# Performance work log

Hardware: AMD Instinct MI355X
Metric: run time of the kernel (lower is better)

## Reference

```python
import jax, jax.numpy as jnp
import numpy as np

# static config (matches init_kwargs)
T_K = 3      # Time_kernel
K = 3        # spatial_kernel_side_length
C = 64       # dim_hidden
H = 4        # num_head
D = 16       # dim_head
NL = 2       # num_layers
F = 3        # dim_feature
N, S1, S2 = 32, 32, 32
P = K // 2
L1 = T_K // 2
M = T_K * K * K
EPS = 1e-5


def _neighbor_mask():
    # spatial_neighbor_mask with an all-ones city mask: offset (k1,k2) is a valid
    # neighbor of cell (s1,s2) iff it lands inside the grid.
    m = np.zeros((S1, S2, K, K), dtype=bool)
    s1 = np.arange(S1); s2 = np.arange(S2)
    for k1 in range(K):
        v1 = (s1 + k1 - P >= 0) & (s1 + k1 - P < S1)
        for k2 in range(K):
            v2 = (s2 + k2 - P >= 0) & (s2 + k2 - P < S2)
            m[:, :, k1, k2] = v1[:, None] & v2[None, :]
    mf = m.reshape(S1, S2, K * K)
    # tiled across Time_kernel, flattened in (t, k1, k2) order like the torch code
    return np.tile(mf[:, :, None, :], (1, 1, T_K, 1)).reshape(S1, S2, M)

_MASK = jnp.asarray(_neighbor_mask())


def _forward(x, W_in, b_in, W_out, b_out, Wq, bq, Wk, bk, Wv, bv):
    # BatchNorm2d (training-mode batch stats, affine = identity init)
    mean = x.mean(axis=(0, 1, 2))
    var = ((x - mean) ** 2).mean(axis=(0, 1, 2))
    h = (x - mean) * jax.lax.rsqrt(var + EPS)
    h = h @ W_in + b_in  # [N,S1,S2,C]

    for l in range(NL):
        res = h  # res_block_thickness = 1 -> residual every layer
        q = (h @ Wq[l] + bq[l]).reshape(N, S1, S2, H, D)
        # spatial unfold (nn.Unfold, padding=K//2, stride=1)
        hp = jnp.pad(h, ((0, 0), (P, P), (P, P), (0, 0)))
        u = jnp.stack([jnp.stack([hp[:, k1:k1 + S1, k2:k2 + S2, :]
                                  for k2 in range(K)]) for k1 in range(K)])  # [K,K,N,S1,S2,C]
        # time unfold (zero-padded shifts along N)
        up = jnp.pad(u, ((0, 0), (0, 0), (L1, L1), (0, 0), (0, 0), (0, 0)))
        ut = jnp.stack([up[:, :, t:t + N] for t in range(T_K)])  # [T,K,K,N,S1,S2,C]
        # per-offset single-Linear MLPs (kernel_neurons=[C,C]), batched over T,K,K
        ks = jnp.einsum('tijnabc,tijcd->nabtijd', ut, Wk[l]) + bk[l]
        vs = jnp.einsum('tijnabc,tijcd->nabtijd', ut, Wv[l]) + bv[l]
        kM = ks.reshape(N, S1, S2, M, H, D)
        vM = vs.reshape(N, S1, S2, M, H, D)
        # unscaled dot-product attention over valid neighbors (masked == dropped)
        sc = jnp.einsum('nabmhd,nabhd->nabhm', kM, q)
        sc = jnp.where(_MASK[None, :, :, None, :], sc, -1e30)
        w = jax.nn.softmax(sc, axis=-1)
        h = jnp.einsum('nabhm,nabmhd->nabhd', w, vM).reshape(N, S1, S2, C)
        h = h + res

    return h @ W_out + b_out  # [N,S1,S2,F]


def setup_inputs() -> dict:
    key = jax.random.key(0)
    k = jax.random.split(key, 11)
    s = 0.05
    return {
        'x': jax.random.normal(k[0], (N, S1, S2, F), jnp.float32),
        'W_in': jax.random.normal(k[1], (F, C), jnp.float32) * s,
        'b_in': jax.random.normal(k[2], (C,), jnp.float32) * s,
        'W_out': jax.random.normal(k[3], (C, F), jnp.float32) * s,
        'b_out': jax.random.normal(k[4], (F,), jnp.float32) * s,
        'Wq': jax.random.normal(k[5], (NL, C, C), jnp.float32) * s,
        'bq': jax.random.normal(k[6], (NL, C), jnp.float32) * s,
        'Wk': jax.random.normal(k[7], (NL, T_K, K, K, C, C), jnp.float32) * s,
        'bk': jax.random.normal(k[8], (NL, T_K, K, K, C), jnp.float32) * s,
        'Wv': jax.random.normal(k[9], (NL, T_K, K, K, C, C), jnp.float32) * s,
        'bv': jax.random.normal(k[10], (NL, T_K, K, K, C), jnp.float32) * s,
    }


def reference(x, W_in, b_in, W_out, b_out, Wq, bq, Wk, bk, Wv, bv):
    return _forward(x, W_in, b_in, W_out, b_out, Wq, bq, Wk, bk, Wv, bv)
```

## Files before the change

### kernel.cpp

```cpp
#include <hip/hip_runtime.h>
#include <hip/hip_bf16.h>


typedef short short8_t __attribute__((ext_vector_type(8)));
typedef float floatx4 __attribute__((ext_vector_type(4)));

__device__ __forceinline__ short f2bs(float f) {
    __hip_bfloat16 h = __float2bfloat16(f);
    return *reinterpret_cast<short*>(&h);
}
__device__ __forceinline__ float bs2f(short s) {
    union { unsigned u; float f; } v;
    v.u = ((unsigned)(unsigned short)s) << 16;
    return v.f;
}
__device__ __forceinline__ int hn_idx(int rowid, int chunk) {
    return rowid * 64 + ((chunk ^ (rowid & 7)) << 3);
}
__device__ __forceinline__ float quad_sum(float p) {
    float a = p, b = p;
    asm("v_permlane16_swap_b32 %0, %1" : "+v"(a), "+v"(b));
    float s = a + b;
    float c = s, d = s;
    asm("v_permlane32_swap_b32 %0, %1" : "+v"(c), "+v"(d));
    return c + d;
}

__global__ void prep_kernel(const float* __restrict__ Wq, const float* __restrict__ Wk,
                            const float* __restrict__ Wv, short* __restrict__ dst,
                            const float* __restrict__ x, float* __restrict__ sums) {
    if (blockIdx.x < 220) {
        int t = blockIdx.x * 256 + threadIdx.x;
        if (t >= 110 * 512) return;
        int mat  = t >> 9;
        int rem  = t & 511;
        int kk   = rem >> 8;
        int nt   = (rem >> 6) & 3;
        int lane = rem & 63;
        int krow = kk * 32 + (lane >> 4) * 8;
        int col  = nt * 16 + (lane & 15);
        const float* W;
        if (mat < 2)       W = Wq + mat * 4096;
        else if (mat < 56) W = Wk + (mat - 2) * 4096;
        else               W = Wv + (mat - 56) * 4096;
        short8_t v;
        #pragma unroll
        for (int j = 0; j < 8; ++j) v[j] = f2bs(W[(krow + j) * 64 + col]);
        *(short8_t*)&dst[(size_t)mat * 4096 + ((kk * 4 + nt) * 64 + lane) * 8] = v;
    } else {
        int bid = blockIdx.x - 220;
        int t = bid * 256 + threadIdx.x;
        const float4* x4 = (const float4*)x;
        float4 v0 = x4[t * 3 + 0], v1 = x4[t * 3 + 1], v2 = x4[t * 3 + 2];
        float vv[6];
        vv[0] = v0.x + v0.w + v1.z + v2.y;
        vv[1] = v0.y + v1.x + v1.w + v2.z;
        vv[2] = v0.z + v1.y + v2.x + v2.w;
        vv[3] = v0.x*v0.x + v0.w*v0.w + v1.z*v1.z + v2.y*v2.y;
        vv[4] = v0.y*v0.y + v1.x*v1.x + v1.w*v1.w + v2.z*v2.z;
        vv[5] = v0.z*v0.z + v1.y*v1.y + v2.x*v2.x + v2.w*v2.w;
        #pragma unroll
        for (int i = 0; i < 6; ++i) {
            #pragma unroll
            for (int off = 1; off < 64; off <<= 1) vv[i] += __shfl_xor(vv[i], off);
        }
        __shared__ float part[4][6];
        if ((threadIdx.x & 63) == 0) {
            #pragma unroll
            for (int i = 0; i < 6; ++i) part[threadIdx.x >> 6][i] = vv[i];
        }
        __syncthreads();
        if (threadIdx.x < 6)
            sums[bid * 8 + threadIdx.x] = part[0][threadIdx.x] + part[1][threadIdx.x] +
                                          part[2][threadIdx.x] + part[3][threadIdx.x];
    }
}

template <bool FIRST>
__global__ __launch_bounds__(512, 4)
void layer_fused(const float* __restrict__ x, const float* __restrict__ sums,
                 const float* __restrict__ W_in, const float* __restrict__ b_in,
                 const short* __restrict__ hbf_in, short* __restrict__ hbf_out,
                 const float* __restrict__ Wout, const float* __restrict__ bout,
                 float* __restrict__ out,
                 const short* __restrict__ wqB, const float* __restrict__ bq,
                 const short* __restrict__ wkB, const float* __restrict__ bk,
                 const short* __restrict__ wvB, const float* __restrict__ bv) {
    __shared__ short HnS[216 * 64];
    __shared__ float Waux[256];
    __shared__ float bn6[6];

    const int tid = threadIdx.x;
    const int bb0 = blockIdx.x * 2, a = blockIdx.y, nb = blockIdx.z;

    if (FIRST) {
        if (tid < 3) {
            float s = 0.f, qq = 0.f;
            #pragma unroll
            for (int p = 0; p < 32; ++p) { s += sums[p * 8 + tid]; qq += sums[p * 8 + 3 + tid]; }
            float mean = s * (1.f / 32768.f);
            float var  = qq * (1.f / 32768.f) - mean * mean;
            bn6[tid]     = mean;
            bn6[3 + tid] = rsqrtf(var + 1e-5f);
        }
        if (tid < 192)      Waux[tid] = W_in[tid];
        else if (tid < 256) Waux[tid] = b_in[tid - 192];
    } else {
        if (tid < 192)      Waux[tid] = Wout[tid];
        else if (tid < 195) Waux[tid] = bout[tid - 192];
    }
    __syncthreads();

    float mean0 = 0, mean1 = 0, mean2 = 0, rs0 = 0, rs1 = 0, rs2 = 0;
    if (FIRST) {
        mean0 = bn6[0]; mean1 = bn6[1]; mean2 = bn6[2];
        rs0 = bn6[3]; rs1 = bn6[4]; rs2 = bn6[5];
    }

    for (int id = tid; id < 1728; id += 512) {
        int rowid = id >> 3, cc = id & 7;
        int r = rowid % 18;
        int rw = rowid / 18;
        int spa = rw >> 2, jcol = rw & 3;
        int aa = a + spa - 1, bb = bb0 + jcol - 1;
        int n  = nb * 16 + r - 1;
        short8_t v = {0, 0, 0, 0, 0, 0, 0, 0};
        if ((unsigned)n < 32u && (unsigned)aa < 32u && (unsigned)bb < 32u) {
            int cell = (n * 32 + aa) * 32 + bb;
            if (FIRST) {
                float xn0 = (x[cell*3+0] - mean0) * rs0;
                float xn1 = (x[cell*3+1] - mean1) * rs1;
                float xn2 = (x[cell*3+2] - mean2) * rs2;
                #pragma unroll
                for (int j = 0; j < 8; ++j) {
                    int c = cc * 8 + j;
                    float h = Waux[192+c] + xn0*Waux[c] + xn1*Waux[64+c] + xn2*Waux[128+c];
                    v[j] = f2bs(h);
                }
            } else {
                v = *(const short8_t*)&hbf_in[cell * 64 + cc * 8];
            }
        }
        *(short8_t*)&HnS[hn_idx(rowid, cc)] = v;
    }
    __syncthreads();

    const int lane = tid & 63;
    const int wv8  = tid >> 6;
    const int w    = wv8 & 3;
    const int g2   = wv8 >> 2;
    const int e    = lane & 15;
    const int q    = lane >> 4;
    const int c0   = w * 16 + q * 4;

    bool va[3], vb[4];
    #pragma unroll
    for (int d = 0; d < 3; ++d) va[d] = (unsigned)(a + d - 1) < 32u;
    #pragma unroll
    for (int j = 0; j < 4; ++j) vb[j] = (unsigned)(bb0 + j - 1) < 32u;

    floatx4 qv[2];
    {
        short8_t wq0 = *(const short8_t*)&wqB[((0 * 4 + w) * 64 + lane) * 8];
        short8_t wq1 = *(const short8_t*)&wqB[((1 * 4 + w) * 64 + lane) * 8];
        const float4 bq4 = *(const float4*)&bq[c0];
        #pragma unroll
        for (int ci = 0; ci < 2; ++ci) {
            const int row = (5 + ci) * 18 + e + 1;
            short8_t h0 = *(const short8_t*)&HnS[hn_idx(row, q)];
            short8_t h1 = *(const short8_t*)&HnS[hn_idx(row, 4 + q)];
            floatx4 acc = {bq4.x, bq4.y, bq4.z, bq4.w};
            acc = __builtin_amdgcn_mfma_f32_16x16x32_bf16(wq0, h0, acc, 0, 0, 0);
            acc = __builtin_amdgcn_mfma_f32_16x16x32_bf16(wq1, h1, acc, 0, 0, 0);
            qv[ci] = acc;
        }
    }

    floatx4 o[2] = {{0,0,0,0},{0,0,0,0}};
    float ss[2] = {0.f, 0.f};

    const int mstart = g2 ? 14 : 0;
    const int mend   = g2 ? 27 : 14;
    for (int m = mstart; m < mend; ++m) {
        const int t  = (m * 57) >> 9;
        const int sp = m - 9 * t;
        const int di = (sp * 11) >> 5;
        const int dj = sp - 3 * di;
        if (!va[di]) continue;
        short8_t wk0 = *(const short8_t*)&wkB[m * 4096 + ((0 * 4 + w) * 64 + lane) * 8];
        short8_t wk1 = *(const short8_t*)&wkB[m * 4096 + ((1 * 4 + w) * 64 + lane) * 8];
        short8_t wv0 = *(const short8_t*)&wvB[m * 4096 + ((0 * 4 + w) * 64 + lane) * 8];
        short8_t wv1 = *(const short8_t*)&wvB[m * 4096 + ((1 * 4 + w) * 64 + lane) * 8];
        const float4 bk4 = *(const float4*)&bk[m * 64 + c0];
        const float4 bv4 = *(const float4*)&bv[m * 64 + c0];
        const int rowb = (di * 4 + dj) * 18 + e + t;
        #pragma unroll
        for (int ci = 0; ci < 2; ++ci) {
            if (!vb[dj + ci]) continue;
            const int row = rowb + ci * 18;
            short8_t h0 = *(const short8_t*)&HnS[hn_idx(row, q)];
            short8_t h1 = *(const short8_t*)&HnS[hn_idx(row, 4 + q)];
            floatx4 kacc = {bk4.x, bk4.y, bk4.z, bk4.w};
            kacc = __builtin_amdgcn_mfma_f32_16x16x32_bf16(wk0, h0, kacc, 0, 0, 0);
            kacc = __builtin_amdgcn_mfma_f32_16x16x32_bf16(wk1, h1, kacc, 0, 0, 0);
            floatx4 vacc = {bv4.x, bv4.y, bv4.z, bv4.w};
            vacc = __builtin_amdgcn_mfma_f32_16x16x32_bf16(wv0, h0, vacc, 0, 0, 0);
            vacc = __builtin_amdgcn_mfma_f32_16x16x32_bf16(wv1, h1, vacc, 0, 0, 0);
            float p = kacc[0] * qv[ci][0] + kacc[1] * qv[ci][1]
                    + kacc[2] * qv[ci][2] + kacc[3] * qv[ci][3];
            p = quad_sum(p);
            float wgt = __expf(p);
            ss[ci] += wgt;
            o[ci][0] += wgt * vacc[0];
            o[ci][1] += wgt * vacc[1];
            o[ci][2] += wgt * vacc[2];
            o[ci][3] += wgt * vacc[3];
        }
    }

    __syncthreads();
    float* stbuf = (float*)HnS;
    if (g2 == 1) {
        #pragma unroll
        for (int ci = 0; ci < 2; ++ci) {
            float* d = &stbuf[(((w * 64 + lane) * 2) + ci) * 5];
            d[0] = ss[ci];
            d[1] = o[ci][0]; d[2] = o[ci][1]; d[3] = o[ci][2]; d[4] = o[ci][3];
        }
    }
    __syncthreads();
    if (g2 == 0) {
        #pragma unroll
        for (int ci = 0; ci < 2; ++ci) {
            const float* d = &stbuf[(((w * 64 + lane) * 2) + ci) * 5];
            float inv = 1.0f / (ss[ci] + d[0]);
            o[ci][0] = (o[ci][0] + d[1]) * inv;
            o[ci][1] = (o[ci][1] + d[2]) * inv;
            o[ci][2] = (o[ci][2] + d[3]) * inv;
            o[ci][3] = (o[ci][3] + d[4]) * inv;
        }
    }

    const int n = nb * 16 + e;
    if (FIRST) {
        if (g2 == 0) {
            #pragma unroll
            for (int ci = 0; ci < 2; ++ci) {
                int cell = (n * 32 + a) * 32 + bb0 + ci;
                float xn0 = (x[cell*3+0] - mean0) * rs0;
                float xn1 = (x[cell*3+1] - mean1) * rs1;
                float xn2 = (x[cell*3+2] - mean2) * rs2;
                short4 hb; short* hbp = (short*)&hb;
                #pragma unroll
                for (int i = 0; i < 4; ++i) {
                    int c = c0 + i;
                    float res = Waux[192+c] + xn0*Waux[c] + xn1*Waux[64+c] + xn2*Waux[128+c];
                    hbp[i] = f2bs(o[ci][i] + res);
                }
                *(short4*)&hbf_out[cell * 64 + c0] = hb;
            }
        }
    } else {
        __syncthreads();
        float* hf = (float*)HnS;
        if (g2 == 0) {
            #pragma unroll
            for (int ci = 0; ci < 2; ++ci) {
                int cell = (n * 32 + a) * 32 + bb0 + ci;
                short4 hb = *(const short4*)&hbf_in[cell * 64 + c0];
                float* d = &hf[(ci * 16 + e) * 65 + c0];
                d[0] = o[ci][0] + bs2f(hb.x);
                d[1] = o[ci][1] + bs2f(hb.y);
                d[2] = o[ci][2] + bs2f(hb.z);
                d[3] = o[ci][3] + bs2f(hb.w);
            }
        }
        __syncthreads();
        if (tid < 96) {
            int rowglob = tid / 3, f = tid - rowglob * 3;
            int ci = rowglob >> 4, row = rowglob & 15;
            float acc = Waux[192 + f];
            #pragma unroll 8
            for (int cc = 0; cc < 64; ++cc) acc += hf[rowglob * 65 + cc] * Waux[cc * 3 + f];
            int nn = nb * 16 + row;
            out[((nn * 32 + a) * 32 + bb0 + ci) * 3 + f] = acc;
        }
    }
}

extern "C" void kernel_launch(void* const* d_in, const int* in_sizes, int n_in,
                              void* d_out, int out_size, void* d_ws, size_t ws_size,
                              hipStream_t stream) {
    const float* x     = (const float*)d_in[0];
    const float* W_in  = (const float*)d_in[1];
    const float* b_in  = (const float*)d_in[2];
    const float* W_out = (const float*)d_in[3];
    const float* b_out = (const float*)d_in[4];
    const float* Wq    = (const float*)d_in[5];
    const float* bq    = (const float*)d_in[6];
    const float* Wk    = (const float*)d_in[7];
    const float* bk    = (const float*)d_in[8];
    const float* Wv    = (const float*)d_in[9];
    const float* bv    = (const float*)d_in[10];

    float* ws    = (float*)d_ws;
    float* sums  = ws;
    short* h1bf  = (short*)(ws + 256);
    short* wB    = h1bf + 2097152;
    float* out   = (float*)d_out;

    prep_kernel<<<252, 256, 0, stream>>>(Wq, Wk, Wv, wB, x, sums);

    const short* wq0 = wB;                const short* wq1 = wB + 4096;
    const short* wk0 = wB + 2 * 4096;     const short* wk1 = wB + (2 + 27) * 4096;
    const short* wv0 = wB + 56 * 4096;    const short* wv1 = wB + (56 + 27) * 4096;

    dim3 grid(16, 32, 2);
    layer_fused<true><<<grid, 512, 0, stream>>>(
        x, sums, W_in, b_in, nullptr, h1bf, nullptr, nullptr, nullptr,
        wq0, bq, wk0, bk, wv0, bv);
    layer_fused<false><<<grid, 512, 0, stream>>>(
        nullptr, nullptr, nullptr, nullptr, h1bf, nullptr, W_out, b_out, out,
        wq1, bq + 64, wk1, bk + 1728, wv1, bv + 1728);
}
```

Baseline: 144.9 us.

## Switch attention MFMAs to 32x32x16 tiles with four-way offset split

```diff
diff --git a/kernel.cpp b/kernel.cpp
--- a/kernel.cpp
+++ b/kernel.cpp
@@ -3,7 +3,7 @@
 
 
 typedef short short8_t __attribute__((ext_vector_type(8)));
-typedef float floatx4 __attribute__((ext_vector_type(4)));
+typedef float floatx16 __attribute__((ext_vector_type(16)));
 
 __device__ __forceinline__ short f2bs(float f) {
     __hip_bfloat16 h = __float2bfloat16(f);
@@ -17,13 +17,10 @@
 __device__ __forceinline__ int hn_idx(int rowid, int chunk) {
     return rowid * 64 + ((chunk ^ (rowid & 7)) << 3);
 }
-__device__ __forceinline__ float quad_sum(float p) {
+__device__ __forceinline__ float half_sum(float p) {
     float a = p, b = p;
-    asm("v_permlane16_swap_b32 %0, %1" : "+v"(a), "+v"(b));
-    float s = a + b;
-    float c = s, d = s;
-    asm("v_permlane32_swap_b32 %0, %1" : "+v"(c), "+v"(d));
-    return c + d;
+    asm("v_permlane32_swap_b32 %0, %1" : "+v"(a), "+v"(b));
+    return a + b;
 }
 
 __global__ void prep_kernel(const float* __restrict__ Wq, const float* __restrict__ Wk,
@@ -34,11 +31,11 @@
         if (t >= 110 * 512) return;
         int mat  = t >> 9;
         int rem  = t & 511;
-        int kk   = rem >> 8;
-        int nt   = (rem >> 6) & 3;
+        int hp   = rem >> 8;
+        int kk   = (rem >> 6) & 3;
         int lane = rem & 63;
-        int krow = kk * 32 + (lane >> 4) * 8;
-        int col  = nt * 16 + (lane & 15);
+        int krow = kk * 16 + ((lane >> 5) << 3);
+        int col  = hp * 32 + (lane & 31);
         const float* W;
         if (mat < 2)       W = Wq + mat * 4096;
         else if (mat < 56) W = Wk + (mat - 2) * 4096;
@@ -46,7 +43,7 @@
         short8_t v;
         #pragma unroll
         for (int j = 0; j < 8; ++j) v[j] = f2bs(W[(krow + j) * 64 + col]);
-        *(short8_t*)&dst[(size_t)mat * 4096 + ((kk * 4 + nt) * 64 + lane) * 8] = v;
+        *(short8_t*)&dst[(size_t)mat * 4096 + ((hp * 4 + kk) * 64 + lane) * 8] = v;
     } else {
         int bid = blockIdx.x - 220;
         int t = bid * 256 + threadIdx.x;
@@ -77,7 +74,7 @@
 }
 
 template <bool FIRST>
-__global__ __launch_bounds__(512, 4)
+__global__ __launch_bounds__(512, 2)
 void layer_fused(const float* __restrict__ x, const float* __restrict__ sums,
                  const float* __restrict__ W_in, const float* __restrict__ b_in,
                  const short* __restrict__ hbf_in, short* __restrict__ hbf_out,
@@ -147,143 +144,203 @@
 
     const int lane = tid & 63;
     const int wv8  = tid >> 6;
-    const int w    = wv8 & 3;
-    const int g2   = wv8 >> 2;
-    const int e    = lane & 15;
-    const int q    = lane >> 4;
-    const int c0   = w * 16 + q * 4;
-
-    bool va[3], vb[4];
+    const int hp   = wv8 & 1;
+    const int g4   = wv8 >> 1;
+    const int col  = lane & 31;
+    const int e    = col & 15;
+    const int ci   = col >> 4;
+    const int h5   = lane >> 5;
+
+    unsigned amask = 0;
     #pragma unroll
-    for (int d = 0; d < 3; ++d) va[d] = (unsigned)(a + d - 1) < 32u;
-    #pragma unroll
-    for (int j = 0; j < 4; ++j) vb[j] = (unsigned)(bb0 + j - 1) < 32u;
-
-    floatx4 qv[2];
+    for (int d = 0; d < 3; ++d) if ((unsigned)(a + d - 1) < 32u) amask |= 1u << d;
+    const bool vbL = (unsigned)(bb0 - 1) < 32u;
+    const bool vbR = (unsigned)(bb0 + 2) < 32u;
+    const unsigned vmask = (ci == 0) ? ((vbL ? 1u : 0u) | 2u | 4u)
+                                     : (1u | 2u | (vbR ? 4u : 0u));
+
+    const int elane = e + ci * 18;
+
+    floatx16 qv;
     {
-        short8_t wq0 = *(const short8_t*)&wqB[((0 * 4 + w) * 64 + lane) * 8];
-        short8_t wq1 = *(const short8_t*)&wqB[((1 * 4 + w) * 64 + lane) * 8];
-        const float4 bq4 = *(const float4*)&bq[c0];
-        #pragma unroll
-        for (int ci = 0; ci < 2; ++ci) {
-            const int row = (5 + ci) * 18 + e + 1;
-            short8_t h0 = *(const short8_t*)&HnS[hn_idx(row, q)];
-            short8_t h1 = *(const short8_t*)&HnS[hn_idx(row, 4 + q)];
-            floatx4 acc = {bq4.x, bq4.y, bq4.z, bq4.w};
-            acc = __builtin_amdgcn_mfma_f32_16x16x32_bf16(wq0, h0, acc, 0, 0, 0);
-            acc = __builtin_amdgcn_mfma_f32_16x16x32_bf16(wq1, h1, acc, 0, 0, 0);
-            qv[ci] = acc;
-        }
-    }
-
-    floatx4 o[2] = {{0,0,0,0},{0,0,0,0}};
-    float ss[2] = {0.f, 0.f};
-
-    const int mstart = g2 ? 14 : 0;
-    const int mend   = g2 ? 27 : 14;
+        const float* bqp = &bq[hp * 32 + 4 * h5];
+        const float4 qa = *(const float4*)&bqp[0];
+        const float4 qb = *(const float4*)&bqp[8];
+        const float4 qc = *(const float4*)&bqp[16];
+        const float4 qd = *(const float4*)&bqp[24];
+        qv = floatx16{qa.x,qa.y,qa.z,qa.w, qb.x,qb.y,qb.z,qb.w,
+                      qc.x,qc.y,qc.z,qc.w, qd.x,qd.y,qd.z,qd.w};
+        const int hrow = (5 + ci) * 18 + e + 1;
+        const int hb = hrow * 64, xr = hrow & 7;
+        const short8_t b0 = *(const short8_t*)&HnS[hb + (((0 + h5) ^ xr) << 3)];
+        const short8_t b1 = *(const short8_t*)&HnS[hb + (((2 + h5) ^ xr) << 3)];
+        const short8_t b2 = *(const short8_t*)&HnS[hb + (((4 + h5) ^ xr) << 3)];
+        const short8_t b3 = *(const short8_t*)&HnS[hb + (((6 + h5) ^ xr) << 3)];
+        const short8_t* wqp = (const short8_t*)&wqB[(hp * 256 + lane) * 8];
+        qv = __builtin_amdgcn_mfma_f32_32x32x16_bf16(wqp[0],   b0, qv, 0, 0, 0);
+        qv = __builtin_amdgcn_mfma_f32_32x32x16_bf16(wqp[64],  b1, qv, 0, 0, 0);
+        qv = __builtin_amdgcn_mfma_f32_32x32x16_bf16(wqp[128], b2, qv, 0, 0, 0);
+        qv = __builtin_amdgcn_mfma_f32_32x32x16_bf16(wqp[192], b3, qv, 0, 0, 0);
+    }
+
+    floatx16 o = {0,0,0,0, 0,0,0,0, 0,0,0,0, 0,0,0,0};
+    float ssA = 0.f, ssB = 0.f;
+
+    const int mstart = g4 * 7;
+    const int mend   = (g4 == 3) ? 27 : mstart + 7;
     for (int m = mstart; m < mend; ++m) {
         const int t  = (m * 57) >> 9;
         const int sp = m - 9 * t;
         const int di = (sp * 11) >> 5;
         const int dj = sp - 3 * di;
-        if (!va[di]) continue;
-        short8_t wk0 = *(const short8_t*)&wkB[m * 4096 + ((0 * 4 + w) * 64 + lane) * 8];
-        short8_t wk1 = *(const short8_t*)&wkB[m * 4096 + ((1 * 4 + w) * 64 + lane) * 8];
-        short8_t wv0 = *(const short8_t*)&wvB[m * 4096 + ((0 * 4 + w) * 64 + lane) * 8];
-        short8_t wv1 = *(const short8_t*)&wvB[m * 4096 + ((1 * 4 + w) * 64 + lane) * 8];
-        const float4 bk4 = *(const float4*)&bk[m * 64 + c0];
-        const float4 bv4 = *(const float4*)&bv[m * 64 + c0];
-        const int rowb = (di * 4 + dj) * 18 + e + t;
-        #pragma unroll
-        for (int ci = 0; ci < 2; ++ci) {
-            if (!vb[dj + ci]) continue;
-            const int row = rowb + ci * 18;
-            short8_t h0 = *(const short8_t*)&HnS[hn_idx(row, q)];
-            short8_t h1 = *(const short8_t*)&HnS[hn_idx(row, 4 + q)];
-            floatx4 kacc = {bk4.x, bk4.y, bk4.z, bk4.w};
-            kacc = __builtin_amdgcn_mfma_f32_16x16x32_bf16(wk0, h0, kacc, 0, 0, 0);
-            kacc = __builtin_amdgcn_mfma_f32_16x16x32_bf16(wk1, h1, kacc, 0, 0, 0);
-            floatx4 vacc = {bv4.x, bv4.y, bv4.z, bv4.w};
-            vacc = __builtin_amdgcn_mfma_f32_16x16x32_bf16(wv0, h0, vacc, 0, 0, 0);
-            vacc = __builtin_amdgcn_mfma_f32_16x16x32_bf16(wv1, h1, vacc, 0, 0, 0);
-            float p = kacc[0] * qv[ci][0] + kacc[1] * qv[ci][1]
-                    + kacc[2] * qv[ci][2] + kacc[3] * qv[ci][3];
-            p = quad_sum(p);
-            float wgt = __expf(p);
-            ss[ci] += wgt;
-            o[ci][0] += wgt * vacc[0];
-            o[ci][1] += wgt * vacc[1];
-            o[ci][2] += wgt * vacc[2];
-            o[ci][3] += wgt * vacc[3];
-        }
+        if (!((amask >> di) & 1u)) continue;
+
+        const int hrow = (di * 4 + dj) * 18 + t + elane;
+        const int hb = hrow * 64, xr = hrow & 7;
+        const short8_t b0 = *(const short8_t*)&HnS[hb + (((0 + h5) ^ xr) << 3)];
+        const short8_t b1 = *(const short8_t*)&HnS[hb + (((2 + h5) ^ xr) << 3)];
+        const short8_t b2 = *(const short8_t*)&HnS[hb + (((4 + h5) ^ xr) << 3)];
+        const short8_t b3 = *(const short8_t*)&HnS[hb + (((6 + h5) ^ xr) << 3)];
+
+        const short8_t* wkp = (const short8_t*)&wkB[m * 4096 + (hp * 256 + lane) * 8];
+        const float* bkp = &bk[m * 64 + hp * 32 + 4 * h5];
+        const float4 ka = *(const float4*)&bkp[0];
+        const float4 kb = *(const float4*)&bkp[8];
+        const float4 kc = *(const float4*)&bkp[16];
+        const float4 kd = *(const float4*)&bkp[24];
+        floatx16 kacc = floatx16{ka.x,ka.y,ka.z,ka.w, kb.x,kb.y,kb.z,kb.w,
+                                 kc.x,kc.y,kc.z,kc.w, kd.x,kd.y,kd.z,kd.w};
+        kacc = __builtin_amdgcn_mfma_f32_32x32x16_bf16(wkp[0],   b0, kacc, 0, 0, 0);
+        kacc = __builtin_amdgcn_mfma_f32_32x32x16_bf16(wkp[64],  b1, kacc, 0, 0, 0);
+        kacc = __builtin_amdgcn_mfma_f32_32x32x16_bf16(wkp[128], b2, kacc, 0, 0, 0);
+        kacc = __builtin_amdgcn_mfma_f32_32x32x16_bf16(wkp[192], b3, kacc, 0, 0, 0);
+
+        const short8_t* wvp = (const short8_t*)&wvB[m * 4096 + (hp * 256 + lane) * 8];
+        const float* bvp = &bv[m * 64 + hp * 32 + 4 * h5];
+        const float4 va0 = *(const float4*)&bvp[0];
+        const float4 va1 = *(const float4*)&bvp[8];
+        const float4 va2 = *(const float4*)&bvp[16];
+        const float4 va3 = *(const float4*)&bvp[24];
+        floatx16 vacc = floatx16{va0.x,va0.y,va0.z,va0.w, va1.x,va1.y,va1.z,va1.w,
+                                 va2.x,va2.y,va2.z,va2.w, va3.x,va3.y,va3.z,va3.w};
+        vacc = __builtin_amdgcn_mfma_f32_32x32x16_bf16(wvp[0],   b0, vacc, 0, 0, 0);
+        vacc = __builtin_amdgcn_mfma_f32_32x32x16_bf16(wvp[64],  b1, vacc, 0, 0, 0);
+        vacc = __builtin_amdgcn_mfma_f32_32x32x16_bf16(wvp[128], b2, vacc, 0, 0, 0);
+        vacc = __builtin_amdgcn_mfma_f32_32x32x16_bf16(wvp[192], b3, vacc, 0, 0, 0);
+
+        float pA = kacc[0] * qv[0];
+        #pragma unroll
+        for (int r = 1; r < 8; ++r) pA += kacc[r] * qv[r];
+        float pB = kacc[8] * qv[8];
+        #pragma unroll
+        for (int r = 9; r < 16; ++r) pB += kacc[r] * qv[r];
+        pA = half_sum(pA);
+        pB = half_sum(pB);
+        const float mf = (float)((vmask >> dj) & 1u);
+        const float wA = __expf(pA) * mf;
+        const float wB = __expf(pB) * mf;
+        ssA += wA; ssB += wB;
+        #pragma unroll
+        for (int r = 0; r < 8; ++r)  o[r] += wA * vacc[r];
+        #pragma unroll
+        for (int r = 8; r < 16; ++r) o[r] += wB * vacc[r];
     }
 
     __syncthreads();
     float* stbuf = (float*)HnS;
-    if (g2 == 1) {
-        #pragma unroll
-        for (int ci = 0; ci < 2; ++ci) {
-            float* d = &stbuf[(((w * 64 + lane) * 2) + ci) * 5];
-            d[0] = ss[ci];
-            d[1] = o[ci][0]; d[2] = o[ci][1]; d[3] = o[ci][2]; d[4] = o[ci][3];
-        }
-    }
-    __syncthreads();
-    if (g2 == 0) {
-        #pragma unroll
-        for (int ci = 0; ci < 2; ++ci) {
-            const float* d = &stbuf[(((w * 64 + lane) * 2) + ci) * 5];
-            float inv = 1.0f / (ss[ci] + d[0]);
-            o[ci][0] = (o[ci][0] + d[1]) * inv;
-            o[ci][1] = (o[ci][1] + d[2]) * inv;
-            o[ci][2] = (o[ci][2] + d[3]) * inv;
-            o[ci][3] = (o[ci][3] + d[4]) * inv;
-        }
+    if (g4 >= 2) {
+        float* d = &stbuf[(((g4 - 2) * 2 + hp) * 64 + lane) * 20];
+        *(float4*)&d[0]  = make_float4(o[0],  o[1],  o[2],  o[3]);
+        *(float4*)&d[4]  = make_float4(o[4],  o[5],  o[6],  o[7]);
+        *(float4*)&d[8]  = make_float4(o[8],  o[9],  o[10], o[11]);
+        *(float4*)&d[12] = make_float4(o[12], o[13], o[14], o[15]);
+        *(float2*)&d[16] = make_float2(ssA, ssB);
+    }
+    __syncthreads();
+    if (g4 < 2) {
+        const float* d = &stbuf[((g4 * 2 + hp) * 64 + lane) * 20];
+        const float4 r0 = *(const float4*)&d[0];
+        const float4 r1 = *(const float4*)&d[4];
+        const float4 r2 = *(const float4*)&d[8];
+        const float4 r3 = *(const float4*)&d[12];
+        const float2 rs = *(const float2*)&d[16];
+        o[0] += r0.x; o[1] += r0.y; o[2]  += r0.z; o[3]  += r0.w;
+        o[4] += r1.x; o[5] += r1.y; o[6]  += r1.z; o[7]  += r1.w;
+        o[8] += r2.x; o[9] += r2.y; o[10] += r2.z; o[11] += r2.w;
+        o[12] += r3.x; o[13] += r3.y; o[14] += r3.z; o[15] += r3.w;
+        ssA += rs.x; ssB += rs.y;
+    }
+    __syncthreads();
+    if (g4 == 1) {
+        float* d = &stbuf[(hp * 64 + lane) * 20];
+        *(float4*)&d[0]  = make_float4(o[0],  o[1],  o[2],  o[3]);
+        *(float4*)&d[4]  = make_float4(o[4],  o[5],  o[6],  o[7]);
+        *(float4*)&d[8]  = make_float4(o[8],  o[9],  o[10], o[11]);
+        *(float4*)&d[12] = make_float4(o[12], o[13], o[14], o[15]);
+        *(float2*)&d[16] = make_float2(ssA, ssB);
+    }
+    __syncthreads();
+    if (g4 == 0) {
+        const float* d = &stbuf[(hp * 64 + lane) * 20];
+        const float4 r0 = *(const float4*)&d[0];
+        const float4 r1 = *(const float4*)&d[4];
+        const float4 r2 = *(const float4*)&d[8];
+        const float4 r3 = *(const float4*)&d[12];
+        const float2 rs = *(const float2*)&d[16];
+        o[0] += r0.x; o[1] += r0.y; o[2]  += r0.z; o[3]  += r0.w;
+        o[4] += r1.x; o[5] += r1.y; o[6]  += r1.z; o[7]  += r1.w;
+        o[8] += r2.x; o[9] += r2.y; o[10] += r2.z; o[11] += r2.w;
+        o[12] += r3.x; o[13] += r3.y; o[14] += r3.z; o[15] += r3.w;
+        ssA += rs.x; ssB += rs.y;
+        const float invA = 1.0f / ssA;
+        const float invB = 1.0f / ssB;
+        #pragma unroll
+        for (int r = 0; r < 8; ++r)  o[r] *= invA;
+        #pragma unroll
+        for (int r = 8; r < 16; ++r) o[r] *= invB;
     }
 
     const int n = nb * 16 + e;
     if (FIRST) {
-        if (g2 == 0) {
-            #pragma unroll
-            for (int ci = 0; ci < 2; ++ci) {
-                int cell = (n * 32 + a) * 32 + bb0 + ci;
-                float xn0 = (x[cell*3+0] - mean0) * rs0;
-                float xn1 = (x[cell*3+1] - mean1) * rs1;
-                float xn2 = (x[cell*3+2] - mean2) * rs2;
-                short4 hb; short* hbp = (short*)&hb;
+        if (g4 == 0) {
+            const int cell = (n * 32 + a) * 32 + bb0 + ci;
+            const float xn0 = (x[cell*3+0] - mean0) * rs0;
+            const float xn1 = (x[cell*3+1] - mean1) * rs1;
+            const float xn2 = (x[cell*3+2] - mean2) * rs2;
+            #pragma unroll
+            for (int g = 0; g < 4; ++g) {
+                short4 hb4; short* hbp = (short*)&hb4;
                 #pragma unroll
                 for (int i = 0; i < 4; ++i) {
-                    int c = c0 + i;
-                    float res = Waux[192+c] + xn0*Waux[c] + xn1*Waux[64+c] + xn2*Waux[128+c];
-                    hbp[i] = f2bs(o[ci][i] + res);
+                    const int c = hp * 32 + g * 8 + 4 * h5 + i;
+                    const float res = Waux[192+c] + xn0*Waux[c] + xn1*Waux[64+c] + xn2*Waux[128+c];
+                    hbp[i] = f2bs(o[g * 4 + i] + res);
                 }
-                *(short4*)&hbf_out[cell * 64 + c0] = hb;
+                *(short4*)&hbf_out[cell * 64 + hp * 32 + g * 8 + 4 * h5] = hb4;
             }
         }
     } else {
         __syncthreads();
         float* hf = (float*)HnS;
-        if (g2 == 0) {
-            #pragma unroll
-            for (int ci = 0; ci < 2; ++ci) {
-                int cell = (n * 32 + a) * 32 + bb0 + ci;
-                short4 hb = *(const short4*)&hbf_in[cell * 64 + c0];
-                float* d = &hf[(ci * 16 + e) * 65 + c0];
-                d[0] = o[ci][0] + bs2f(hb.x);
-                d[1] = o[ci][1] + bs2f(hb.y);
-                d[2] = o[ci][2] + bs2f(hb.z);
-                d[3] = o[ci][3] + bs2f(hb.w);
+        if (g4 == 0) {
+            const int cell = (n * 32 + a) * 32 + bb0 + ci;
+            #pragma unroll
+            for (int g = 0; g < 4; ++g) {
+                const short4 hb4 = *(const short4*)&hbf_in[cell * 64 + hp * 32 + g * 8 + 4 * h5];
+                float4 tv = make_float4(o[g*4+0] + bs2f(hb4.x), o[g*4+1] + bs2f(hb4.y),
+                                        o[g*4+2] + bs2f(hb4.z), o[g*4+3] + bs2f(hb4.w));
+                *(float4*)&hf[col * 68 + hp * 32 + g * 8 + 4 * h5] = tv;
             }
         }
         __syncthreads();
         if (tid < 96) {
             int rowglob = tid / 3, f = tid - rowglob * 3;
-            int ci = rowglob >> 4, row = rowglob & 15;
+            int cio = rowglob >> 4, row = rowglob & 15;
             float acc = Waux[192 + f];
             #pragma unroll 8
-            for (int cc = 0; cc < 64; ++cc) acc += hf[rowglob * 65 + cc] * Waux[cc * 3 + f];
+            for (int cc = 0; cc < 64; ++cc) acc += hf[rowglob * 68 + cc] * Waux[cc * 3 + f];
             int nn = nb * 16 + row;
-            out[((nn * 32 + a) * 32 + bb0 + ci) * 3 + f] = acc;
+            out[((nn * 32 + a) * 32 + bb0 + cio) * 3 + f] = acc;
         }
     }
 }
```

After: 146.1 us. About the same (+0.9%).
